# Kernel optimization log

Measured on AMD Instinct MI355X. Metric: run time of the kernel, lower is better.

## Reference

```python
import jax, jax.numpy as jnp
import numpy as np


def setup_inputs() -> dict:
    key = jax.random.key(0)
    ks = jax.random.split(key, 6)
    B_, S, D_in, D_out, R, E = 4, 2048, 2048, 2048, 64, 16
    x = jax.random.normal(ks[0], (B_, S, D_in), dtype=jnp.float32)
    W_base = jax.random.normal(ks[1], (D_out, D_in), dtype=jnp.float32) * (D_in ** -0.5)
    b_base = jax.random.normal(ks[2], (D_out,), dtype=jnp.float32) * 0.02
    # orthogonal rows, as get_orthogonal_matrix(reservoir_size, in_features)
    G = np.asarray(jax.random.normal(ks[3], (D_in, R), dtype=jnp.float32))
    Q, _ = np.linalg.qr(G)  # [D_in, R] orthonormal columns
    A = jnp.asarray(Q.T, dtype=jnp.float32)  # [R, D_in]
    # B initialized to zeros in the module; use small random so delta is nontrivial
    Bmat = jax.random.normal(ks[4], (E, D_out, R), dtype=jnp.float32) * 0.02
    W_router = jax.random.normal(ks[5], (E, D_in), dtype=jnp.float32) * 0.02
    return {"x": x, "W_base": W_base, "b_base": b_base, "A": A, "B": Bmat,
            "W_router": W_router, "top_k": 2}


def reference(x, W_base, b_base, A, B, W_router, top_k):
    E = W_router.shape[0]
    base_output = jnp.einsum('bsi,oi->bso', x, W_base) + b_base          # [B,S,D_out]
    res_hidden = jnp.einsum('bsi,ri->bsr', x, A)                          # [B,S,R]
    router_logits = jnp.einsum('bsi,ei->bse', x, W_router)                # [B,S,E]
    routing_weights = jax.nn.softmax(router_logits, axis=-1)
    if top_k > 0 and top_k < E:
        _, top_idx = jax.lax.top_k(routing_weights, top_k)                # [B,S,k]
        mask = jax.nn.one_hot(top_idx, E, dtype=routing_weights.dtype).sum(axis=-2)
        routing_weights = routing_weights * mask
        routing_weights = routing_weights / (routing_weights.sum(axis=-1, keepdims=True) + 1e-6)
    # contract experts+rank without materializing [B,S,E,D_out]
    h = jnp.einsum('bsr,bse->bser', res_hidden, routing_weights)          # [B,S,E,R] (small)
    delta = jnp.einsum('bser,edr->bsd', h, B)                             # [B,S,D_out]
    return base_output + delta
```

## Files before the change

### kernel.cpp

```cpp
#include <hip/hip_runtime.h>
#include <hip/hip_bf16.h>

#define D_IN  2048
#define D_OUT 2048
#define RNK   64
#define NE    16
#define KTOT  3072
#define NTILE 48

typedef __attribute__((ext_vector_type(8))) short bf16x8;
typedef __attribute__((ext_vector_type(4))) float f32x4;
typedef __attribute__((ext_vector_type(16))) float f32x16;

__device__ __forceinline__ void async_ld16(const void* g, void* l) {
    __builtin_amdgcn_global_load_lds(
        (const __attribute__((address_space(1))) void*)g,
        (__attribute__((address_space(3))) void*)l,
        16, 0, 0);
}

__global__ __launch_bounds__(384) void castwa_kernel(
    const float* __restrict__ Wb, const float* __restrict__ Bm,
    const float* __restrict__ A,
    __hip_bfloat16* __restrict__ Wc, __hip_bfloat16* __restrict__ Ab)
{
    const int c = threadIdx.x * 8;
    const float* src;
    __hip_bfloat16* dst;
    if (blockIdx.x < D_OUT) {
        const int n = blockIdx.x;
        if (c < D_IN) {
            src = Wb + (size_t)n * D_IN + c;
        } else {
            const int j = c - D_IN;
            const int e = j >> 6, r = j & 63;
            src = Bm + ((size_t)e * D_OUT + n) * RNK + r;
        }
        dst = Wc + (size_t)n * KTOT + c;
    } else {
        if (c >= D_IN) return;
        const int r = blockIdx.x - D_OUT;
        src = A + (size_t)r * D_IN + c;
        dst = Ab + (size_t)r * D_IN + c;
    }
    const float4 a = *(const float4*)src;
    const float4 b = *(const float4*)(src + 4);
    const float vv[8] = {a.x, a.y, a.z, a.w, b.x, b.y, b.z, b.w};
    union { bf16x8 v; __hip_bfloat16 h[8]; } u;
#pragma unroll
    for (int q = 0; q < 8; ++q) u.h[q] = __float2bfloat16(vv[q]);
    *(bf16x8*)dst = u.v;
}

__global__ __launch_bounds__(512) void prep2_kernel(
    const float* __restrict__ x, const float* __restrict__ Wr,
    const __hip_bfloat16* __restrict__ Ab,
    const int* __restrict__ topk_p, __hip_bfloat16* __restrict__ Xc)
{
    __shared__ __align__(16) char smem[81920];
    __hip_bfloat16* xb = (__hip_bfloat16*)smem;
    float* stg = (float*)(smem + 65536);
    float* red = (float*)smem;
    float* wf  = (float*)(smem + 65536);

    const int tid = threadIdx.x;
    const int wave = tid >> 6, lane = tid & 63;
    const int l31 = lane & 31, lh = lane >> 5;
    const int qm = lane & 15, quad = lane >> 4;
    const int t0 = blockIdx.x * 16;
    const int tl = wave * 2 + lh;
    const size_t myt = (size_t)t0 + tl;

    float acc[NE];
#pragma unroll
    for (int e = 0; e < NE; ++e) acc[e] = 0.f;

    const float4* x4 = (const float4*)x;
    const int sg = l31 ^ ((l31 >> 3) & 7);
    const float* wr_src = Wr + (size_t)tl * D_IN + sg * 4;

    async_ld16(wr_src, (void*)(stg + wave * 256));
    float4 xv = x4[myt * 512 + l31];
    float4 xn;

    for (int c = 0; c < 16; ++c) {
        asm volatile("s_waitcnt vmcnt(1)" ::: "memory");
        __builtin_amdgcn_sched_barrier(0);
        __builtin_amdgcn_s_barrier();
        __builtin_amdgcn_sched_barrier(0);
        if (c < 15) {
            async_ld16(wr_src + (c + 1) * 128,
                       (void*)(stg + ((c + 1) & 1) * 2048 + wave * 256));
            xn = x4[myt * 512 + (c + 1) * 32 + l31];
        }
        union { short4 v; __hip_bfloat16 h[4]; } u;
        u.h[0] = __float2bfloat16(xv.x); u.h[1] = __float2bfloat16(xv.y);
        u.h[2] = __float2bfloat16(xv.z); u.h[3] = __float2bfloat16(xv.w);
        *(short4*)(Xc + myt * KTOT + c * 128 + l31 * 4) = u.v;
        const int G = c * 16 + (l31 >> 1);
        *(short4*)((char*)xb + tl * 4096 + ((G ^ (tl & 7)) * 16)
                   + (l31 & 1) * 8) = u.v;
        const float* sb = stg + (c & 1) * 2048;
#pragma unroll
        for (int e = 0; e < NE; ++e) {
            const float4 wv = *(const float4*)(sb + e * 128 + sg * 4);
            acc[e] += xv.x * wv.x + xv.y * wv.y + xv.z * wv.z + xv.w * wv.w;
        }
        if (c < 15) xv = xn;
    }

#pragma unroll
    for (int off = 16; off; off >>= 1)
#pragma unroll
        for (int e = 0; e < NE; ++e)
            acc[e] += __shfl_xor(acc[e], off, 64);
    if (l31 == 0) {
        const int k = topk_p[0];
        float m = -1e30f;
#pragma unroll
        for (int e = 0; e < NE; ++e) m = fmaxf(m, acc[e]);
        float w[NE]; float ssum = 0.f;
#pragma unroll
        for (int e = 0; e < NE; ++e) { w[e] = __expf(acc[e] - m); ssum += w[e]; }
        const float inv = 1.f / ssum;
#pragma unroll
        for (int e = 0; e < NE; ++e) w[e] *= inv;
        float* wfout = wf + (size_t)tl * NE;
        if (k > 0 && k < NE) {
            int chosen[NE];
#pragma unroll
            for (int e = 0; e < NE; ++e) chosen[e] = 0;
            float ksum = 0.f;
            for (int it = 0; it < k; ++it) {
                int bi = 0; float bv = -1.f;
                for (int e = 0; e < NE; ++e)
                    if (!chosen[e] && w[e] > bv) { bv = w[e]; bi = e; }
                chosen[bi] = 1; ksum += bv;
            }
            const float rinv = 1.f / (ksum + 1e-6f);
            for (int e = 0; e < NE; ++e) wfout[e] = chosen[e] ? w[e] * rinv : 0.f;
        } else {
            for (int e = 0; e < NE; ++e) wfout[e] = w[e];
        }
    }
    __syncthreads();

    f32x4 racc[4] = {};
    const int kb = wave * 256;
#pragma unroll
    for (int s = 0; s < 4; ++s) {
        const int k0 = kb + s * 64;
        const int gg0 = (k0 >> 3) + quad;
        const bf16x8 a0 = *(const bf16x8*)((char*)xb + qm * 4096 + ((gg0 ^ (qm & 7)) * 16));
        const bf16x8 a1 = *(const bf16x8*)((char*)xb + qm * 4096 + (((gg0 + 4) ^ (qm & 7)) * 16));
        bf16x8 b0[4], b1[4];
#pragma unroll
        for (int nf = 0; nf < 4; ++nf) {
            const __hip_bfloat16* bp = Ab + (size_t)(qm + nf * 16) * D_IN + k0 + quad * 8;
            b0[nf] = *(const bf16x8*)bp;
            b1[nf] = *(const bf16x8*)(bp + 32);
        }
#pragma unroll
        for (int nf = 0; nf < 4; ++nf) {
            racc[nf] = __builtin_amdgcn_mfma_f32_16x16x32_bf16(a0, b0[nf], racc[nf], 0, 0, 0);
            racc[nf] = __builtin_amdgcn_mfma_f32_16x16x32_bf16(a1, b1[nf], racc[nf], 0, 0, 0);
        }
    }
    __syncthreads();

#pragma unroll
    for (int nf = 0; nf < 4; ++nf)
#pragma unroll
        for (int r = 0; r < 4; ++r)
            red[(wave * 16 + quad * 4 + r) * 64 + nf * 16 + qm] = racc[nf][r];
    __syncthreads();

#pragma unroll
    for (int it = 0; it < 4; ++it) {
        const int s = it * 512 + tid;
        const int t = s >> 7;
        const int chunk = s & 127;
        const int e = chunk >> 3, r0 = (chunk & 7) * 8;
        const float wgt = wf[t * 16 + e];
        float4 s0 = {0.f, 0.f, 0.f, 0.f}, s1 = {0.f, 0.f, 0.f, 0.f};
#pragma unroll
        for (int w2 = 0; w2 < 8; ++w2) {
            const float4 p0 = ((const float4*)red)[(w2 * 16 + t) * 16 + (r0 >> 2)];
            const float4 p1 = ((const float4*)red)[(w2 * 16 + t) * 16 + (r0 >> 2) + 1];
            s0.x += p0.x; s0.y += p0.y; s0.z += p0.z; s0.w += p0.w;
            s1.x += p1.x; s1.y += p1.y; s1.z += p1.z; s1.w += p1.w;
        }
        union { bf16x8 v; __hip_bfloat16 h[8]; } u;
        u.h[0] = __float2bfloat16(wgt * s0.x); u.h[1] = __float2bfloat16(wgt * s0.y);
        u.h[2] = __float2bfloat16(wgt * s0.z); u.h[3] = __float2bfloat16(wgt * s0.w);
        u.h[4] = __float2bfloat16(wgt * s1.x); u.h[5] = __float2bfloat16(wgt * s1.y);
        u.h[6] = __float2bfloat16(wgt * s1.z); u.h[7] = __float2bfloat16(wgt * s1.w);
        *(bf16x8*)(Xc + (size_t)(t0 + t) * KTOT + D_IN + chunk * 8) = u.v;
    }
}

#define LDA3(BUF, M, ks) (*(const bf16x8*)(smem + (BUF) + \
    ((((M) >> 1) * 128 + wm2 * 64 + ((M) & 1) * 32 + l31) * 128) + \
    (((((ks) * 2 + lhi) ^ (l31 & 7))) << 4)))
#define LDB3(BUF, N, ks) (*(const bf16x8*)(smem + 65536 + (BUF) + \
    ((wn4 * 64 + (N) * 32 + l31) * 128) + \
    (((((ks) * 2 + lhi) ^ (l31 & 7))) << 4)))

#define GP(BUF, MH, ISSUE, WAIT) do { \
    bf16x8 af[2][4]; \
    if ((MH) == 0) { \
        _Pragma("unroll") for (int n = 0; n < 2; ++n) \
        _Pragma("unroll") for (int ks = 0; ks < 4; ++ks) \
            bfr[n][ks] = LDB3(BUF, n, ks); \
    } \
    _Pragma("unroll") for (int m = 0; m < 2; ++m) \
    _Pragma("unroll") for (int ks = 0; ks < 4; ++ks) \
        af[m][ks] = LDA3(BUF, (MH) * 2 + m, ks); \
    ISSUE; \
    WAIT; \
    __builtin_amdgcn_sched_barrier(0); \
    __builtin_amdgcn_s_barrier(); \
    asm volatile("s_waitcnt lgkmcnt(0)" ::: "memory"); \
    __builtin_amdgcn_sched_barrier(0); \
    __builtin_amdgcn_s_setprio(1); \
    _Pragma("unroll") for (int ks = 0; ks < 4; ++ks) \
    _Pragma("unroll") for (int m = 0; m < 2; ++m) \
    _Pragma("unroll") for (int n = 0; n < 2; ++n) \
        acc[(MH) * 2 + m][n] = __builtin_amdgcn_mfma_f32_32x32x16_bf16( \
            af[m][ks], bfr[n][ks], acc[(MH) * 2 + m][n], 0, 0, 0); \
    __builtin_amdgcn_s_setprio(0); \
    __builtin_amdgcn_sched_barrier(0); \
    __builtin_amdgcn_s_barrier(); \
    __builtin_amdgcn_sched_barrier(0); \
} while (0)

__global__ __launch_bounds__(512, 1) void gemm5_kernel(
    const __hip_bfloat16* __restrict__ Am,
    const __hip_bfloat16* __restrict__ Bm,
    const float* __restrict__ bias,
    float* __restrict__ C)
{
    __shared__ __align__(16) char smem[131072];
    const int tid = threadIdx.x;
    const int w = tid >> 6, lane = tid & 63;
    const int l31 = lane & 31, lhi = lane >> 5;
    const int wm2 = w >> 2, wn4 = w & 3;

    const int flat = blockIdx.y * gridDim.x + blockIdx.x;
    const int xcd = flat & 7, j = flat >> 3;
    const int bm = (xcd & 3) * 8 + (j & 7);
    const int bn = (xcd >> 2) * 4 + (j >> 3);

    const int rb0 = w * 16 + (lane >> 3);
    const int rb1 = rb0 + 8;
    const int gs0 = (lane & 7) ^ (rb0 & 7);
    const int gs1 = (lane & 7) ^ (rb1 & 7);
    const __hip_bfloat16* pA0 = Am + (size_t)(bm * 256 + rb0) * KTOT + gs0 * 8;
    const __hip_bfloat16* pA1 = Am + (size_t)(bm * 256 + rb1) * KTOT + gs1 * 8;
    const __hip_bfloat16* pB0 = Bm + (size_t)(bn * 256 + rb0) * KTOT + gs0 * 8;
    const __hip_bfloat16* pB1 = Bm + (size_t)(bn * 256 + rb1) * KTOT + gs1 * 8;
    const size_t HO = (size_t)128 * KTOT;

    f32x16 acc[4][2] = {};
    bf16x8 bfr[2][4];

    auto stageP1 = [&](int tn) {
        const size_t ko = (size_t)tn * 64;
        char* da = smem + (tn & 1) * 32768 + w * 2048;
        async_ld16(pA0 + ko, da);
        async_ld16(pA1 + ko, da + 1024);
        char* db = smem + 65536 + (tn & 1) * 32768 + w * 2048;
        async_ld16(pB0 + ko, db);
        async_ld16(pB1 + ko, db + 1024);
        async_ld16(pB0 + HO + ko, db + 16384);
        async_ld16(pB1 + HO + ko, db + 16384 + 1024);
    };
    auto stageP2 = [&](int tn) {
        const size_t ko = (size_t)tn * 64;
        char* da = smem + (tn & 1) * 32768 + 16384 + w * 2048;
        async_ld16(pA0 + HO + ko, da);
        async_ld16(pA1 + HO + ko, da + 1024);
    };

    stageP1(0); stageP2(0); stageP1(1);
    asm volatile("s_waitcnt vmcnt(8)" ::: "memory");
    __builtin_amdgcn_sched_barrier(0);
    __builtin_amdgcn_s_barrier();
    __builtin_amdgcn_sched_barrier(0);

    for (int t = 0; t < NTILE - 2; ++t) {
        const int bo = (t & 1) * 32768;
        GP(bo, 0, stageP2(t + 1),
           asm volatile("s_waitcnt vmcnt(8)" ::: "memory"));
        GP(bo, 1, stageP1(t + 2),
           asm volatile("s_waitcnt vmcnt(8)" ::: "memory"));
    }
    {
        const int bo = ((NTILE - 2) & 1) * 32768;
        GP(bo, 0, stageP2(NTILE - 1),
           asm volatile("s_waitcnt vmcnt(8)" ::: "memory"));
        GP(bo, 1, ,
           asm volatile("s_waitcnt vmcnt(2)" ::: "memory"));
    }
    {
        const int bo = ((NTILE - 1) & 1) * 32768;
        GP(bo, 0, ,
           asm volatile("s_waitcnt vmcnt(0)" ::: "memory"));
        GP(bo, 1, , );
    }

#pragma unroll
    for (int n = 0; n < 2; ++n) {
        const int col = bn * 256 + wn4 * 64 + n * 32 + l31;
        const float bbv = bias[col];
#pragma unroll
        for (int m = 0; m < 4; ++m) {
            const size_t rbase = (size_t)bm * 256 + (m >> 1) * 128 + wm2 * 64
                               + (m & 1) * 32 + 4 * lhi;
#pragma unroll
            for (int reg = 0; reg < 16; ++reg) {
                const size_t row = rbase + (reg & 3) + 8 * (reg >> 2);
                C[row * D_OUT + col] = acc[m][n][reg] + bbv;
            }
        }
    }
}

extern "C" void kernel_launch(void* const* d_in, const int* in_sizes, int n_in,
                              void* d_out, int out_size, void* d_ws, size_t ws_size,
                              hipStream_t stream) {
    const float* x    = (const float*)d_in[0];
    const float* Wb   = (const float*)d_in[1];
    const float* bb   = (const float*)d_in[2];
    const float* A    = (const float*)d_in[3];
    const float* Bm   = (const float*)d_in[4];
    const float* Wr   = (const float*)d_in[5];
    const int*   topk = (const int*)d_in[6];
    float* out = (float*)d_out;
    const int T = in_sizes[0] / D_IN;

    __hip_bfloat16* Xc = (__hip_bfloat16*)d_ws;
    __hip_bfloat16* Wc = (__hip_bfloat16*)((char*)d_ws + (size_t)T * KTOT * 2);
    __hip_bfloat16* Ab = (__hip_bfloat16*)d_out;

    castwa_kernel<<<D_OUT + RNK, 384, 0, stream>>>(Wb, Bm, A, Wc, Ab);
    prep2_kernel<<<T / 16, 512, 0, stream>>>(x, Wr, Ab, topk, Xc);
    gemm5_kernel<<<dim3(32, 8), 512, 0, stream>>>(Xc, Wc, bb, out);
}
```

Measured before the change: 265.5 us.

## Move router logits and top-k into the weight-cast kernel as extra blocks

Router logit computation, softmax and top-k selection move out of the x-cast kernel into extra blocks appended to the weight-cast launch. Those blocks stage x and W_router tiles through a triple-buffered async LDS pipeline and write the routing weights to a scratch area in the output buffer. The x-cast/res-hidden kernel then only converts x to bf16 and reads the precomputed routing weights. The aim is to overlap routing work with the weight-cast blocks and to shorten the second kernel. The cost is that x is read twice from global memory, and the scratch region in the output buffer must not overlap anything still in use.

```diff
diff --git a/kernel.cpp b/kernel.cpp
--- a/kernel.cpp
+++ b/kernel.cpp
@@ -19,47 +19,144 @@
         16, 0, 0);
 }
 
-__global__ __launch_bounds__(384) void castwa_kernel(
+__global__ __launch_bounds__(384) void wprep_kernel(
     const float* __restrict__ Wb, const float* __restrict__ Bm,
-    const float* __restrict__ A,
-    __hip_bfloat16* __restrict__ Wc, __hip_bfloat16* __restrict__ Ab)
+    const float* __restrict__ A,  const float* __restrict__ x,
+    const float* __restrict__ Wr, const int* __restrict__ topk_p,
+    __hip_bfloat16* __restrict__ Wc, __hip_bfloat16* __restrict__ Ab,
+    float* __restrict__ wfin)
 {
-    const int c = threadIdx.x * 8;
-    const float* src;
-    __hip_bfloat16* dst;
-    if (blockIdx.x < D_OUT) {
-        const int n = blockIdx.x;
-        if (c < D_IN) {
-            src = Wb + (size_t)n * D_IN + c;
+    __shared__ __align__(16) float xs[3][16 * 128];
+    __shared__ __align__(16) float ws[3][16 * 128];
+    __shared__ float lg[NE * 16];
+
+    if (blockIdx.x < D_OUT + RNK) {
+        const int c = threadIdx.x * 8;
+        const float* src;
+        __hip_bfloat16* dst;
+        if (blockIdx.x < D_OUT) {
+            const int n = blockIdx.x;
+            if (c < D_IN) {
+                src = Wb + (size_t)n * D_IN + c;
+            } else {
+                const int j = c - D_IN;
+                const int e = j >> 6, r = j & 63;
+                src = Bm + ((size_t)e * D_OUT + n) * RNK + r;
+            }
+            dst = Wc + (size_t)n * KTOT + c;
         } else {
-            const int j = c - D_IN;
-            const int e = j >> 6, r = j & 63;
-            src = Bm + ((size_t)e * D_OUT + n) * RNK + r;
-        }
-        dst = Wc + (size_t)n * KTOT + c;
-    } else {
-        if (c >= D_IN) return;
-        const int r = blockIdx.x - D_OUT;
-        src = A + (size_t)r * D_IN + c;
-        dst = Ab + (size_t)r * D_IN + c;
-    }
-    const float4 a = *(const float4*)src;
-    const float4 b = *(const float4*)(src + 4);
-    const float vv[8] = {a.x, a.y, a.z, a.w, b.x, b.y, b.z, b.w};
-    union { bf16x8 v; __hip_bfloat16 h[8]; } u;
-#pragma unroll
-    for (int q = 0; q < 8; ++q) u.h[q] = __float2bfloat16(vv[q]);
-    *(bf16x8*)dst = u.v;
-}
-
-__global__ __launch_bounds__(512) void prep2_kernel(
-    const float* __restrict__ x, const float* __restrict__ Wr,
-    const __hip_bfloat16* __restrict__ Ab,
-    const int* __restrict__ topk_p, __hip_bfloat16* __restrict__ Xc)
+            if (c >= D_IN) return;
+            const int r = blockIdx.x - D_OUT;
+            src = A + (size_t)r * D_IN + c;
+            dst = Ab + (size_t)r * D_IN + c;
+        }
+        const float4 a = *(const float4*)src;
+        const float4 b = *(const float4*)(src + 4);
+        const float vv[8] = {a.x, a.y, a.z, a.w, b.x, b.y, b.z, b.w};
+        union { bf16x8 v; __hip_bfloat16 h[8]; } u;
+#pragma unroll
+        for (int q = 0; q < 8; ++q) u.h[q] = __float2bfloat16(vv[q]);
+        *(bf16x8*)dst = u.v;
+        return;
+    }
+
+    const int t0 = (blockIdx.x - (D_OUT + RNK)) * 16;
+    const int tid = threadIdx.x;
+    const int wave = tid >> 6, lane = tid & 63;
+    const int tok = tid & 15, e = tid >> 4;
+    float acc = 0.f;
+
+    auto stage = [&](int c) {
+        if (wave < 4) {
+            const int half = wave & 1;
+            const float* base = (wave < 2) ? (x + (size_t)t0 * D_IN) : Wr;
+            float* dstb = (wave < 2) ? xs[c % 3] : ws[c % 3];
+#pragma unroll
+            for (int i = 0; i < 4; ++i) {
+                const int row = half * 8 + i * 2 + (lane >> 5);
+                async_ld16(base + (size_t)row * D_IN + c * 128 + (lane & 31) * 4,
+                           (void*)(dstb + (half * 8 + i * 2) * 128));
+            }
+        }
+    };
+
+    stage(0); stage(1);
+    for (int c = 0; c < 15; ++c) {
+        asm volatile("s_waitcnt vmcnt(4)" ::: "memory");
+        __builtin_amdgcn_sched_barrier(0);
+        __builtin_amdgcn_s_barrier();
+        __builtin_amdgcn_sched_barrier(0);
+        if (c < 14) stage(c + 2);
+        if (tid < 256) {
+            const float* xr = xs[c % 3] + tok * 128;
+            const float* wr = ws[c % 3] + e * 128;
+#pragma unroll
+            for (int jj = 0; jj < 32; ++jj) {
+                const int j4 = ((jj + tok) & 31) * 4;
+                const float4 xv = *(const float4*)(xr + j4);
+                const float4 wv = *(const float4*)(wr + j4);
+                acc += xv.x * wv.x + xv.y * wv.y + xv.z * wv.z + xv.w * wv.w;
+            }
+        }
+    }
+    {
+        asm volatile("s_waitcnt vmcnt(0)" ::: "memory");
+        __builtin_amdgcn_sched_barrier(0);
+        __builtin_amdgcn_s_barrier();
+        __builtin_amdgcn_sched_barrier(0);
+        if (tid < 256) {
+            const float* xr = xs[15 % 3] + tok * 128;
+            const float* wr = ws[15 % 3] + e * 128;
+#pragma unroll
+            for (int jj = 0; jj < 32; ++jj) {
+                const int j4 = ((jj + tok) & 31) * 4;
+                const float4 xv = *(const float4*)(xr + j4);
+                const float4 wv = *(const float4*)(wr + j4);
+                acc += xv.x * wv.x + xv.y * wv.y + xv.z * wv.z + xv.w * wv.w;
+            }
+        }
+    }
+    if (tid < 256) lg[e * 16 + tok] = acc;
+    __syncthreads();
+
+    if (tid < 16) {
+        const int k = topk_p[0];
+        float m = -1e30f;
+        float w[NE];
+#pragma unroll
+        for (int ee = 0; ee < NE; ++ee) { w[ee] = lg[ee * 16 + tid]; m = fmaxf(m, w[ee]); }
+        float ssum = 0.f;
+#pragma unroll
+        for (int ee = 0; ee < NE; ++ee) { w[ee] = __expf(w[ee] - m); ssum += w[ee]; }
+        const float inv = 1.f / ssum;
+#pragma unroll
+        for (int ee = 0; ee < NE; ++ee) w[ee] *= inv;
+        float* wfout = wfin + (size_t)(t0 + tid) * NE;
+        if (k > 0 && k < NE) {
+            int chosen[NE];
+#pragma unroll
+            for (int ee = 0; ee < NE; ++ee) chosen[ee] = 0;
+            float ksum = 0.f;
+            for (int it = 0; it < k; ++it) {
+                int bi = 0; float bv = -1.f;
+                for (int ee = 0; ee < NE; ++ee)
+                    if (!chosen[ee] && w[ee] > bv) { bv = w[ee]; bi = ee; }
+                chosen[bi] = 1; ksum += bv;
+            }
+            const float rinv = 1.f / (ksum + 1e-6f);
+            for (int ee = 0; ee < NE; ++ee) wfout[ee] = chosen[ee] ? w[ee] * rinv : 0.f;
+        } else {
+            for (int ee = 0; ee < NE; ++ee) wfout[ee] = w[ee];
+        }
+    }
+}
+
+__global__ __launch_bounds__(512) void cast_rh_kernel(
+    const float* __restrict__ x, const __hip_bfloat16* __restrict__ Ab,
+    const float* __restrict__ wfin, __hip_bfloat16* __restrict__ Xc)
 {
-    __shared__ __align__(16) char smem[81920];
+    __shared__ __align__(16) char smem[66560];
     __hip_bfloat16* xb = (__hip_bfloat16*)smem;
-    float* stg = (float*)(smem + 65536);
     float* red = (float*)smem;
     float* wf  = (float*)(smem + 65536);
 
@@ -71,28 +168,11 @@
     const int tl = wave * 2 + lh;
     const size_t myt = (size_t)t0 + tl;
 
-    float acc[NE];
-#pragma unroll
-    for (int e = 0; e < NE; ++e) acc[e] = 0.f;
-
     const float4* x4 = (const float4*)x;
-    const int sg = l31 ^ ((l31 >> 3) & 7);
-    const float* wr_src = Wr + (size_t)tl * D_IN + sg * 4;
-
-    async_ld16(wr_src, (void*)(stg + wave * 256));
-    float4 xv = x4[myt * 512 + l31];
-    float4 xn;
-
+
+#pragma unroll
     for (int c = 0; c < 16; ++c) {
-        asm volatile("s_waitcnt vmcnt(1)" ::: "memory");
-        __builtin_amdgcn_sched_barrier(0);
-        __builtin_amdgcn_s_barrier();
-        __builtin_amdgcn_sched_barrier(0);
-        if (c < 15) {
-            async_ld16(wr_src + (c + 1) * 128,
-                       (void*)(stg + ((c + 1) & 1) * 2048 + wave * 256));
-            xn = x4[myt * 512 + (c + 1) * 32 + l31];
-        }
+        const float4 xv = x4[myt * 512 + c * 32 + l31];
         union { short4 v; __hip_bfloat16 h[4]; } u;
         u.h[0] = __float2bfloat16(xv.x); u.h[1] = __float2bfloat16(xv.y);
         u.h[2] = __float2bfloat16(xv.z); u.h[3] = __float2bfloat16(xv.w);
@@ -100,49 +180,9 @@
         const int G = c * 16 + (l31 >> 1);
         *(short4*)((char*)xb + tl * 4096 + ((G ^ (tl & 7)) * 16)
                    + (l31 & 1) * 8) = u.v;
-        const float* sb = stg + (c & 1) * 2048;
-#pragma unroll
-        for (int e = 0; e < NE; ++e) {
-            const float4 wv = *(const float4*)(sb + e * 128 + sg * 4);
-            acc[e] += xv.x * wv.x + xv.y * wv.y + xv.z * wv.z + xv.w * wv.w;
-        }
-        if (c < 15) xv = xn;
-    }
-
-#pragma unroll
-    for (int off = 16; off; off >>= 1)
-#pragma unroll
-        for (int e = 0; e < NE; ++e)
-            acc[e] += __shfl_xor(acc[e], off, 64);
-    if (l31 == 0) {
-        const int k = topk_p[0];
-        float m = -1e30f;
-#pragma unroll
-        for (int e = 0; e < NE; ++e) m = fmaxf(m, acc[e]);
-        float w[NE]; float ssum = 0.f;
-#pragma unroll
-        for (int e = 0; e < NE; ++e) { w[e] = __expf(acc[e] - m); ssum += w[e]; }
-        const float inv = 1.f / ssum;
-#pragma unroll
-        for (int e = 0; e < NE; ++e) w[e] *= inv;
-        float* wfout = wf + (size_t)tl * NE;
-        if (k > 0 && k < NE) {
-            int chosen[NE];
-#pragma unroll
-            for (int e = 0; e < NE; ++e) chosen[e] = 0;
-            float ksum = 0.f;
-            for (int it = 0; it < k; ++it) {
-                int bi = 0; float bv = -1.f;
-                for (int e = 0; e < NE; ++e)
-                    if (!chosen[e] && w[e] > bv) { bv = w[e]; bi = e; }
-                chosen[bi] = 1; ksum += bv;
-            }
-            const float rinv = 1.f / (ksum + 1e-6f);
-            for (int e = 0; e < NE; ++e) wfout[e] = chosen[e] ? w[e] * rinv : 0.f;
-        } else {
-            for (int e = 0; e < NE; ++e) wfout[e] = w[e];
-        }
-    }
+    }
+    if (tid < 64)
+        ((float4*)wf)[tid] = ((const float4*)(wfin + (size_t)t0 * NE))[tid];
     __syncthreads();
 
     f32x4 racc[4] = {};
@@ -342,8 +382,10 @@
     __hip_bfloat16* Xc = (__hip_bfloat16*)d_ws;
     __hip_bfloat16* Wc = (__hip_bfloat16*)((char*)d_ws + (size_t)T * KTOT * 2);
     __hip_bfloat16* Ab = (__hip_bfloat16*)d_out;
-
-    castwa_kernel<<<D_OUT + RNK, 384, 0, stream>>>(Wb, Bm, A, Wc, Ab);
-    prep2_kernel<<<T / 16, 512, 0, stream>>>(x, Wr, Ab, topk, Xc);
+    float* wfin = (float*)d_out + 8 * 1024 * 1024;
+
+    wprep_kernel<<<D_OUT + RNK + T / 16, 384, 0, stream>>>(
+        Wb, Bm, A, x, Wr, topk, Wc, Ab, wfin);
+    cast_rh_kernel<<<T / 16, 512, 0, stream>>>(x, Ab, wfin, Xc);
     gemm5_kernel<<<dim3(32, 8), 512, 0, stream>>>(Xc, Wc, bb, out);
 }
```

After: 280.2 us. 1.06x slower.
